# Kernel optimization log

Measured on AMD Instinct MI355X. Metric: run time of the kernel, lower is better.

## Reference

```python
import jax, jax.numpy as jnp
import numpy as np

B, T, DP, DQ, DO = 128, 2048, 256, 256, 256


def setup_inputs() -> dict:
    key = jax.random.key(0)
    ks = jax.random.split(key, 10)
    return {
        "input_p": jax.random.normal(ks[0], (B, DP), dtype=jnp.float32),
        "mask_p": jnp.ones((B,), dtype=jnp.float32),
        "input_q": jax.random.normal(ks[1], (B, T, DQ), dtype=jnp.float32),
        "mask_q": jax.random.randint(ks[2], (B, T), 0, 2, dtype=jnp.int32),
        "h_tm1": jax.random.normal(ks[3], (B, DO), dtype=jnp.float32),
        # layer-0 parameters (depth == 0)
        "W_p_r": jax.random.normal(ks[4], (DO, DP + DO), dtype=jnp.float32) * 0.04,
        "b_p_r": jnp.zeros((DO,), dtype=jnp.float32),
        "W_q": jax.random.normal(ks[5], (DO, DQ), dtype=jnp.float32) * 0.05,
        "b_q": jnp.zeros((DO,), dtype=jnp.float32),
        "w": jax.random.normal(ks[6], (DO,), dtype=jnp.float32) * 0.05,
        "match_b": jnp.ones((1,), dtype=jnp.float32),
        "depth": 0,
    }


def masked_softmax(x, m, axis=-1):
    x = jnp.clip(x, -15.0, 15.0)
    x = x * m
    e_x = jnp.exp(x - jnp.max(x, axis=axis, keepdims=True))
    e_x = e_x * m
    return e_x / (jnp.sum(e_x, axis=axis, keepdims=True) + 1e-6)


def reference(input_p, mask_p, input_q, mask_q, h_tm1, W_p_r, b_p_r, W_q, b_q, w, match_b, depth):
    mq = mask_q.astype(jnp.float32)
    # G_p_r: [B, 1, DO]
    G_p_r = (jnp.concatenate([input_p, h_tm1], axis=-1) @ W_p_r.T + b_p_r)[:, None, :]
    # G_q: [B, T, DO]
    G_q = input_q @ W_q.T + b_q
    G = jnp.tanh(G_p_r + G_q)
    alpha = jnp.einsum("btd,d->bt", G, w) + match_b  # [B, T]
    alpha = masked_softmax(alpha, mq, axis=-1)
    z = jnp.einsum("bt,btd->bd", alpha, input_q)  # bmm context
    return jnp.concatenate([input_p, z], axis=1)  # [B, DP+DQ]
```

## Files before the change

kernel.cpp:

```cpp
#include <hip/hip_runtime.h>

typedef short short8 __attribute__((ext_vector_type(8)));
typedef float floatx4 __attribute__((ext_vector_type(4)));

constexpr int Bn = 128, Tn = 2048, DPn = 256, DQn = 256, DOn = 256;
constexpr int NCH = Tn / 64;

__device__ inline unsigned short f2bf(float x) {
    unsigned u = __float_as_uint(x);
    u += 0x7fffu + ((u >> 16) & 1u);
    return (unsigned short)(u >> 16);
}
__device__ inline float bf2f(unsigned short h) {
    return __uint_as_float(((unsigned)h) << 16);
}
__device__ inline float fast_tanh(float x) {
    float e = __expf(2.0f * x);
    return 1.0f - 2.0f / (e + 1.0f);
}

__global__ __launch_bounds__(256) void cvt_wq_kernel(const float* __restrict__ wq,
                                                     unsigned short* __restrict__ wqbf) {
    int idx = blockIdx.x * 256 + threadIdx.x;
    float4 v = ((const float4*)wq)[idx];
    unsigned p0 = (unsigned)f2bf(v.x) | ((unsigned)f2bf(v.y) << 16);
    unsigned p1 = (unsigned)f2bf(v.z) | ((unsigned)f2bf(v.w) << 16);
    ((uint2*)wqbf)[idx] = make_uint2(p0, p1);
}

__global__ __launch_bounds__(256) void base_kernel(const float* __restrict__ input_p,
                                                   const float* __restrict__ h_tm1,
                                                   const float* __restrict__ Wpr,
                                                   const float* __restrict__ bpr,
                                                   const float* __restrict__ bq,
                                                   float* __restrict__ base) {
    __shared__ float v[512];
    int b = blockIdx.x, tid = threadIdx.x;
    v[tid]       = input_p[b * DPn + tid];
    v[256 + tid] = h_tm1[b * DOn + tid];
    __syncthreads();
    const float4* row = (const float4*)(Wpr + (size_t)tid * 512);
    const float4* vv  = (const float4*)v;
    float acc = 0.f;
#pragma unroll 8
    for (int i = 0; i < 128; i++) {
        float4 r = row[i], x = vv[i];
        acc = fmaf(r.x, x.x, acc);
        acc = fmaf(r.y, x.y, acc);
        acc = fmaf(r.z, x.z, acc);
        acc = fmaf(r.w, x.w, acc);
    }
    base[b * DOn + tid] = acc + bpr[tid] + bq[tid];
}

__global__ __launch_bounds__(256, 2) void fused_kernel(const float* __restrict__ q,
                                                       const unsigned short* __restrict__ wqbf,
                                                       const float* __restrict__ base,
                                                       const float* __restrict__ wvec,
                                                       const float* __restrict__ matchb,
                                                       const int* __restrict__ maskq,
                                                       float* __restrict__ zpart,
                                                       float* __restrict__ spart,
                                                       float* __restrict__ mpart) {
    __shared__ unsigned short qtile[32 * 64 * 8];
    __shared__ float partl[4][64];
    __shared__ float earr[64];
    __shared__ float zp[4][256];

    int b = blockIdx.y, c = blockIdx.x;
    int t0 = c * 64;
    int tid = threadIdx.x;
    int w = tid >> 6, lane = tid & 63, l15 = lane & 15, quad = lane >> 4;

    short8 bfr[4][8];
    const unsigned short* bbase = wqbf + (size_t)(w * 64 + l15) * 256 + quad * 8;
#pragma unroll
    for (int nt = 0; nt < 4; nt++)
#pragma unroll
        for (int ks = 0; ks < 8; ks++)
            bfr[nt][ks] = *(const short8*)(bbase + nt * 16 * 256 + ks * 32);
    float bn[4], wn[4];
#pragma unroll
    for (int nt = 0; nt < 4; nt++) {
        int n = w * 64 + nt * 16 + l15;
        bn[nt] = base[b * DOn + n];
        wn[nt] = wvec[n];
    }

    {
        const float* src = q + ((size_t)b * Tn + t0 + w * 16 + l15) * DQn + quad * 8;
        unsigned short* dst = qtile + ((size_t)(w * 8) * 64 + lane) * 8;
#pragma unroll
        for (int ks = 0; ks < 8; ks++) {
            float4 v0 = *(const float4*)(src + ks * 32);
            float4 v1 = *(const float4*)(src + ks * 32 + 4);
            short8 s;
            s[0] = (short)f2bf(v0.x); s[1] = (short)f2bf(v0.y);
            s[2] = (short)f2bf(v0.z); s[3] = (short)f2bf(v0.w);
            s[4] = (short)f2bf(v1.x); s[5] = (short)f2bf(v1.y);
            s[6] = (short)f2bf(v1.z); s[7] = (short)f2bf(v1.w);
            *(short8*)(dst + ks * 512) = s;
        }
    }
    __syncthreads();

#pragma unroll
    for (int mt = 0; mt < 4; mt++) {
        short8 af[8];
        const unsigned short* ab = qtile + ((size_t)(mt * 8) * 64 + lane) * 8;
#pragma unroll
        for (int ks = 0; ks < 8; ks++) af[ks] = *(const short8*)(ab + ks * 512);
        float prow[4] = {0.f, 0.f, 0.f, 0.f};
#pragma unroll
        for (int nt = 0; nt < 4; nt++) {
            floatx4 acc = {0.f, 0.f, 0.f, 0.f};
#pragma unroll
            for (int ks = 0; ks < 8; ks++)
                acc = __builtin_amdgcn_mfma_f32_16x16x32_bf16(af[ks], bfr[nt][ks], acc, 0, 0, 0);
#pragma unroll
            for (int r = 0; r < 4; r++) {
                float g = fast_tanh(acc[r] + bn[nt]);
                prow[r] = fmaf(g, wn[nt], prow[r]);
            }
        }
#pragma unroll
        for (int off = 1; off < 16; off <<= 1)
#pragma unroll
            for (int r = 0; r < 4; r++) prow[r] += __shfl_xor(prow[r], off);
        if (l15 == 0) {
#pragma unroll
            for (int r = 0; r < 4; r++) partl[w][mt * 16 + quad * 4 + r] = prow[r];
        }
    }
    __syncthreads();

    if (tid < 64) {
        int t = tid;
        float lg = partl[0][t] + partl[1][t] + partl[2][t] + partl[3][t] + matchb[0];
        float m = (float)maskq[(size_t)b * Tn + t0 + t];
        float x = fminf(fmaxf(lg, -15.f), 15.f) * m;
        float e = __expf(x - 15.f) * m;
        earr[t] = e;
        float xm = x, es = e;
#pragma unroll
        for (int off = 1; off < 64; off <<= 1) {
            xm = fmaxf(xm, __shfl_xor(xm, off));
            es += __shfl_xor(es, off);
        }
        if (t == 0) {
            mpart[b * NCH + c] = xm;
            spart[b * NCH + c] = es;
        }
    }
    __syncthreads();

    float et = earr[w * 16 + l15];
#pragma unroll
    for (int i = 0; i < 8; i++) {
        short8 f = *(const short8*)(qtile + ((size_t)(w * 8 + i) * 64 + lane) * 8);
        float v[8];
#pragma unroll
        for (int j = 0; j < 8; j++) v[j] = bf2f((unsigned short)f[j]) * et;
#pragma unroll
        for (int off = 1; off < 16; off <<= 1)
#pragma unroll
            for (int j = 0; j < 8; j++) v[j] += __shfl_xor(v[j], off);
        if (l15 == 0) {
            float* zd = &zp[w][i * 32 + quad * 8];
            *(float4*)(zd)     = make_float4(v[0], v[1], v[2], v[3]);
            *(float4*)(zd + 4) = make_float4(v[4], v[5], v[6], v[7]);
        }
    }
    __syncthreads();

    {
        int d = tid;
        float zs = zp[0][d] + zp[1][d] + zp[2][d] + zp[3][d];
        zpart[((size_t)b * NCH + c) * DQn + d] = zs;
    }
}

__global__ __launch_bounds__(256) void final_kernel(const float* __restrict__ input_p,
                                                    const float* __restrict__ zpart,
                                                    const float* __restrict__ spart,
                                                    const float* __restrict__ mpart,
                                                    float* __restrict__ out) {
    int b = blockIdx.x, tid = threadIdx.x;
    float S = 0.f, mx = -1e30f;
#pragma unroll 8
    for (int c = 0; c < NCH; c++) {
        S += spart[b * NCH + c];
        mx = fmaxf(mx, mpart[b * NCH + c]);
    }
    float denom = S + 1e-6f * __expf(mx - 15.f);
    float inv = 1.0f / denom;
    float zs = 0.f;
#pragma unroll 8
    for (int c = 0; c < NCH; c++) zs += zpart[((size_t)b * NCH + c) * DQn + tid];
    out[(size_t)b * 512 + tid] = input_p[(size_t)b * DPn + tid];
    out[(size_t)b * 512 + 256 + tid] = zs * inv;
}

extern "C" void kernel_launch(void* const* d_in, const int* in_sizes, int n_in,
                              void* d_out, int out_size, void* d_ws, size_t ws_size,
                              hipStream_t stream) {
    const float* input_p = (const float*)d_in[0];
    const float* input_q = (const float*)d_in[2];
    const int*   mask_q  = (const int*)d_in[3];
    const float* h_tm1   = (const float*)d_in[4];
    const float* W_p_r   = (const float*)d_in[5];
    const float* b_p_r   = (const float*)d_in[6];
    const float* W_q     = (const float*)d_in[7];
    const float* b_q     = (const float*)d_in[8];
    const float* w       = (const float*)d_in[9];
    const float* match_b = (const float*)d_in[10];
    float* out = (float*)d_out;

    char* ws = (char*)d_ws;
    unsigned short* wqbf = (unsigned short*)ws;
    float* base  = (float*)(ws + 131072);
    float* zpart = (float*)(ws + 262144);
    float* spart = (float*)(ws + 262144 + 4194304);
    float* mpart = (float*)(ws + 262144 + 4194304 + 16384);

    cvt_wq_kernel<<<64, 256, 0, stream>>>(W_q, wqbf);
    base_kernel<<<Bn, 256, 0, stream>>>(input_p, h_tm1, W_p_r, b_p_r, b_q, base);
    fused_kernel<<<dim3(NCH, Bn), 256, 0, stream>>>(input_q, wqbf, base, w, match_b,
                                                    mask_q, zpart, spart, mpart);
    final_kernel<<<Bn, 256, 0, stream>>>(input_p, zpart, spart, mpart, out);
}
```

Baseline: 452.0 us.

## Compute context from fp32 global reload instead of bf16 tile shuffle reduction

The weighted context sum now re-reads the fp32 query rows from global memory (likely cache-resident), with each half-wave accumulating 8 rows directly. A small shared-memory reduction over 8 groups replaces the per-element xor-shuffle reduction over bf16 values. The bf16 tile's shared buffer is reused for the partial sums, and float-to-bf16 packing uses the hardware paired conversion intrinsic. This trades many shuffles for extra global/L2 reads and also raises the precision of z.

Result: faster. 439.2 us (-2.8%).

```diff
diff --git a/kernel.cpp b/kernel.cpp
--- a/kernel.cpp
+++ b/kernel.cpp
@@ -1,4 +1,5 @@
 #include <hip/hip_runtime.h>
+#include <hip/hip_bf16.h>
 
 typedef short short8 __attribute__((ext_vector_type(8)));
 typedef float floatx4 __attribute__((ext_vector_type(4)));
@@ -6,13 +7,9 @@
 constexpr int Bn = 128, Tn = 2048, DPn = 256, DQn = 256, DOn = 256;
 constexpr int NCH = Tn / 64;
 
-__device__ inline unsigned short f2bf(float x) {
-    unsigned u = __float_as_uint(x);
-    u += 0x7fffu + ((u >> 16) & 1u);
-    return (unsigned short)(u >> 16);
-}
-__device__ inline float bf2f(unsigned short h) {
-    return __uint_as_float(((unsigned)h) << 16);
+__device__ inline unsigned pk2(float x, float y) {
+    __hip_bfloat162 h = __float22bfloat162_rn(make_float2(x, y));
+    return *(unsigned*)&h;
 }
 __device__ inline float fast_tanh(float x) {
     float e = __expf(2.0f * x);
@@ -23,9 +20,7 @@
                                                      unsigned short* __restrict__ wqbf) {
     int idx = blockIdx.x * 256 + threadIdx.x;
     float4 v = ((const float4*)wq)[idx];
-    unsigned p0 = (unsigned)f2bf(v.x) | ((unsigned)f2bf(v.y) << 16);
-    unsigned p1 = (unsigned)f2bf(v.z) | ((unsigned)f2bf(v.w) << 16);
-    ((uint2*)wqbf)[idx] = make_uint2(p0, p1);
+    ((uint2*)wqbf)[idx] = make_uint2(pk2(v.x, v.y), pk2(v.z, v.w));
 }
 
 __global__ __launch_bounds__(256) void base_kernel(const float* __restrict__ input_p,
@@ -62,10 +57,10 @@
                                                        float* __restrict__ zpart,
                                                        float* __restrict__ spart,
                                                        float* __restrict__ mpart) {
-    __shared__ unsigned short qtile[32 * 64 * 8];
+    __shared__ __align__(16) char shraw[32 * 64 * 16];
+    unsigned short* qtile = (unsigned short*)shraw;
     __shared__ float partl[4][64];
     __shared__ float earr[64];
-    __shared__ float zp[4][256];
 
     int b = blockIdx.y, c = blockIdx.x;
     int t0 = c * 64;
@@ -94,12 +89,12 @@
         for (int ks = 0; ks < 8; ks++) {
             float4 v0 = *(const float4*)(src + ks * 32);
             float4 v1 = *(const float4*)(src + ks * 32 + 4);
-            short8 s;
-            s[0] = (short)f2bf(v0.x); s[1] = (short)f2bf(v0.y);
-            s[2] = (short)f2bf(v0.z); s[3] = (short)f2bf(v0.w);
-            s[4] = (short)f2bf(v1.x); s[5] = (short)f2bf(v1.y);
-            s[6] = (short)f2bf(v1.z); s[7] = (short)f2bf(v1.w);
-            *(short8*)(dst + ks * 512) = s;
+            uint4 u;
+            u.x = pk2(v0.x, v0.y);
+            u.y = pk2(v0.z, v0.w);
+            u.z = pk2(v1.x, v1.y);
+            u.w = pk2(v1.z, v1.w);
+            *(uint4*)(dst + ks * 512) = u;
         }
     }
     __syncthreads();
@@ -154,29 +149,36 @@
     }
     __syncthreads();
 
-    float et = earr[w * 16 + l15];
-#pragma unroll
-    for (int i = 0; i < 8; i++) {
-        short8 f = *(const short8*)(qtile + ((size_t)(w * 8 + i) * 64 + lane) * 8);
-        float v[8];
-#pragma unroll
-        for (int j = 0; j < 8; j++) v[j] = bf2f((unsigned short)f[j]) * et;
-#pragma unroll
-        for (int off = 1; off < 16; off <<= 1)
-#pragma unroll
-            for (int j = 0; j < 8; j++) v[j] += __shfl_xor(v[j], off);
-        if (l15 == 0) {
-            float* zd = &zp[w][i * 32 + quad * 8];
-            *(float4*)(zd)     = make_float4(v[0], v[1], v[2], v[3]);
-            *(float4*)(zd + 4) = make_float4(v[4], v[5], v[6], v[7]);
-        }
-    }
-    __syncthreads();
-
     {
-        int d = tid;
-        float zs = zp[0][d] + zp[1][d] + zp[2][d] + zp[3][d];
-        zpart[((size_t)b * NCH + c) * DQn + d] = zs;
+        int o = lane & 31, h = lane >> 5, g = w * 2 + h;
+        const float* qz = q + ((size_t)b * Tn + t0 + g * 8) * DQn + o * 8;
+        float acc[8] = {0.f, 0.f, 0.f, 0.f, 0.f, 0.f, 0.f, 0.f};
+#pragma unroll
+        for (int s = 0; s < 8; s++) {
+            float e = earr[g * 8 + s];
+            float4 a0 = *(const float4*)(qz + (size_t)s * DQn);
+            float4 a1 = *(const float4*)(qz + (size_t)s * DQn + 4);
+            acc[0] = fmaf(e, a0.x, acc[0]);
+            acc[1] = fmaf(e, a0.y, acc[1]);
+            acc[2] = fmaf(e, a0.z, acc[2]);
+            acc[3] = fmaf(e, a0.w, acc[3]);
+            acc[4] = fmaf(e, a1.x, acc[4]);
+            acc[5] = fmaf(e, a1.y, acc[5]);
+            acc[6] = fmaf(e, a1.z, acc[6]);
+            acc[7] = fmaf(e, a1.w, acc[7]);
+        }
+        float* zp = (float*)shraw;
+        float* zrow = zp + g * 256 + o * 8;
+        *(float4*)(zrow)     = make_float4(acc[0], acc[1], acc[2], acc[3]);
+        *(float4*)(zrow + 4) = make_float4(acc[4], acc[5], acc[6], acc[7]);
+    }
+    __syncthreads();
+    {
+        const float* zp = (const float*)shraw;
+        float zs = 0.f;
+#pragma unroll
+        for (int r = 0; r < 8; r++) zs += zp[r * 256 + tid];
+        zpart[((size_t)b * NCH + c) * DQn + tid] = zs;
     }
 }
 
```
